# Optimization experiments

Hardware: AMD Instinct MI355X
Metric: run time of the kernel (lower is better)

Reference implementation:

```python
import jax, jax.numpy as jnp
import numpy as np

NEG_SLOPE = 0.2
EPS = 1e-16


def _add_self_loops(edge_index, edge_weight, N):
    # PyG add_self_loops with fill_value='mean': self-loop attr = mean of
    # incoming edge attrs per node (0 if node has no incoming edges).
    src, dst = edge_index[0], edge_index[1]
    ones = jnp.ones_like(edge_weight)
    cnt = jax.ops.segment_sum(ones, dst, num_segments=N)
    wsum = jax.ops.segment_sum(edge_weight, dst, num_segments=N)
    self_w = jnp.where(cnt > 0, wsum / jnp.maximum(cnt, 1.0), 0.0)
    loop = jnp.arange(N, dtype=src.dtype)
    return (jnp.concatenate([src, loop]), jnp.concatenate([dst, loop]),
            jnp.concatenate([edge_weight, self_w]))


def _gatv2_layer(x, src, dst, ew, Wl, Wr, att, We, bias, N):
    # x: [M, N, Din]; src/dst: [E']; ew: [E']; att: [H, C]
    M = x.shape[0]
    H, C = att.shape
    xl = (x @ Wl).reshape(M, N, H, C)   # source transform (lin_l)
    xr = (x @ Wr).reshape(M, N, H, C)   # target transform (lin_r)
    xj = xl[:, src]                      # [M, E', H, C] gather source feats
    xi = xr[:, dst]                      # [M, E', H, C] gather target feats
    ee = (ew[:, None] @ We).reshape(-1, H, C)  # [E', H, C] edge embedding
    s = jax.nn.leaky_relu(xi + xj + ee[None], NEG_SLOPE)
    logits = jnp.einsum('mehc,hc->meh', s, att)  # [M, E', H]
    # segment softmax over edges grouped by destination node
    smax = jax.vmap(lambda u: jax.ops.segment_max(u, dst, num_segments=N))(logits)
    a = jnp.exp(logits - smax[:, dst])
    denom = jax.vmap(lambda u: jax.ops.segment_sum(u, dst, num_segments=N))(a)
    alpha = a / (denom[:, dst] + EPS)
    msg = alpha[..., None] * xj          # [M, E', H, C]
    out = jax.vmap(lambda u: jax.ops.segment_sum(u, dst, num_segments=N))(msg)
    return out.reshape(M, N, H * C) + bias


def setup_inputs() -> dict:
    key = jax.random.key(0)
    ks = jax.random.split(key, 14)
    B, T, N, Din = 2, 8, 5000, 64
    E, H, OUT = 80000, 2, 128
    C = OUT // H  # 64
    g = jax.nn.initializers.glorot_uniform()
    inp = {
        'x': jax.random.normal(ks[0], (B, T, N, Din), jnp.float32),
        'edge_index': jax.random.randint(ks[1], (2, E), 0, N, jnp.int32),
        'edge_weight': jax.random.uniform(ks[2], (E,), jnp.float32),
        # conv1 params
        'Wl1': g(ks[3], (Din, H * C), jnp.float32),
        'Wr1': g(ks[4], (Din, H * C), jnp.float32),
        'att1': g(ks[5], (H, C), jnp.float32),
        'We1': g(ks[6], (1, H * C), jnp.float32),
        'b1': jnp.zeros((H * C,), jnp.float32),
        # conv2 params
        'Wl2': g(ks[7], (OUT, H * C), jnp.float32),
        'Wr2': g(ks[8], (OUT, H * C), jnp.float32),
        'att2': g(ks[9], (H, C), jnp.float32),
        'We2': g(ks[10], (1, H * C), jnp.float32),
        'b2': jnp.zeros((H * C,), jnp.float32),
    }
    return inp


def reference(x, edge_index, edge_weight, Wl1, Wr1, att1, We1, b1,
              Wl2, Wr2, att2, We2, b2):
    B, T, N, Din = x.shape
    M = B * T
    # Tiling edges by B*T with node offsets is equivalent to sharing the same
    # edge list across M independent graph copies -> vectorize over M.
    src, dst, ew = _add_self_loops(edge_index, edge_weight, N)
    h = x.reshape(M, N, Din)
    h = _gatv2_layer(h, src, dst, ew, Wl1, Wr1, att1, We1, b1, N)
    h = jax.nn.elu(h)
    h = _gatv2_layer(h, src, dst, ew, Wl2, Wr2, att2, We2, b2, N)
    h = jax.nn.elu(h)
    return h.reshape(B, T, N, -1)
```

## Files before the change

### kernel.cpp

```cpp
#include <hip/hip_runtime.h>
#include <cstdint>
#include <cstddef>

static constexpr float NEG_SLOPE_C = 0.2f;
static constexpr float EPS_C = 1e-16f;
static constexpr float LOG2E_C = 1.4426950408889634f;

#if defined(__has_builtin)
#if __has_builtin(__builtin_amdgcn_exp2f)
#define EXP2F(x) __builtin_amdgcn_exp2f(x)
#else
#define EXP2F(x) exp2f(x)
#endif
#else
#define EXP2F(x) exp2f(x)
#endif

typedef __attribute__((ext_vector_type(8))) short bf16x8;
typedef __attribute__((ext_vector_type(4))) float f32x4;

__device__ __forceinline__ short bf16_rne(float x) {
    unsigned u = __float_as_uint(x);
    u = (u + 0x7FFF + ((u >> 16) & 1)) >> 16;
    return (short)u;
}
__device__ __forceinline__ float bf16f(short s) {
    return __uint_as_float(((unsigned)(unsigned short)s) << 16);
}

template<int CTRL>
__device__ __forceinline__ float dpp_add_f(float v) {
    int x = __builtin_amdgcn_update_dpp(0, __float_as_int(v), CTRL, 0xf, 0xf, true);
    return v + __int_as_float(x);
}

__device__ __forceinline__ float reduce16(float q) {
    q = dpp_add_f<0xB1>(q);
    q = dpp_add_f<0x4E>(q);
    q = dpp_add_f<0x141>(q);
    q = dpp_add_f<0x140>(q);
    return q;
}


__global__ void degree_kernel(const int* __restrict__ ei, const float* __restrict__ ew,
                              int E, int* __restrict__ cnt, float* __restrict__ wsum) {
    int e = blockIdx.x * blockDim.x + threadIdx.x;
    if (e >= E) return;
    int dst = ei[E + e];
    atomicAdd(&cnt[dst], 1);
    atomicAdd(&wsum[dst], ew[e]);
}

__global__ void scan_kernel(const int* __restrict__ cnt, const float* __restrict__ wsum,
                            int N, int E, int* __restrict__ offs, float* __restrict__ self_w) {
    __shared__ int bufA[1024];
    __shared__ int bufB[1024];
    int t = threadIdx.x;
    int chunk = (N + 1023) / 1024;
    int lo = t * chunk;
    int hi = lo + chunk; if (hi > N) hi = N; if (lo > N) lo = N;
    int s = 0;
    for (int n = lo; n < hi; ++n) s += cnt[n];
    bufA[t] = s;
    __syncthreads();
    int* srcb = bufA; int* dstb = bufB;
    for (int d = 1; d < 1024; d <<= 1) {
        int v = srcb[t];
        if (t >= d) v += srcb[t - d];
        dstb[t] = v;
        __syncthreads();
        int* tmp = srcb; srcb = dstb; dstb = tmp;
    }
    int run = (t == 0) ? 0 : srcb[t - 1];
    for (int n = lo; n < hi; ++n) { offs[n] = run; run += cnt[n]; }
    if (t == 0) offs[N] = E;
    for (int n = t; n < N; n += 1024) {
        int c = cnt[n];
        self_w[n] = (c > 0) ? (wsum[n] / (float)c) : 0.0f;
    }
}

__global__ void scatter_kernel(const int* __restrict__ ei, const float* __restrict__ ew, int E,
                               const int* __restrict__ offs, int* __restrict__ cursor,
                               int2* __restrict__ pairs) {
    int e = blockIdx.x * blockDim.x + threadIdx.x;
    if (e >= E) return;
    int dst = ei[E + e];
    int pos = offs[dst] + atomicAdd(&cursor[dst], 1);
    pairs[pos] = make_int2(ei[e], __float_as_int(ew[e]));
}


template<int K>
__global__ void wprep_kernel(const float* __restrict__ Wl, const float* __restrict__ Wr,
                             uint4* __restrict__ Wf) {
    const int gid = blockIdx.x * 256 + threadIdx.x;
    const int lane = gid & 63;
    const int t = (gid >> 6) & 15;
    const int s = gid >> 10;
    const int mr = lane & 15, q = lane >> 4;
    const int col = t * 16 + mr;
    const float* src = (col < 128) ? (Wl + col) : (Wr + col - 128);
    union { short sh[8]; uint4 u; } hv, lv;
    #pragma unroll
    for (int j = 0; j < 8; ++j) {
        const float v = src[(size_t)(s * 32 + q * 8 + j) * 128];
        const short h = bf16_rne(v);
        hv.sh[j] = h;
        lv.sh[j] = bf16_rne(v - bf16f(h));
    }
    const size_t base = (size_t)s * 2048 + (size_t)(t * 2) * 64 + lane;
    Wf[base] = hv.u;
    Wf[base + 64] = lv.u;
}


template<int K>
__global__ __launch_bounds__(256) void gemm_mfma_kernel(
    const float* __restrict__ X, const uint4* __restrict__ Wf,
    float* __restrict__ outL, float* __restrict__ outR) {
    __shared__ uint4 wbuf[2048];
    const int tid = threadIdx.x;
    const int wv = tid >> 6;
    const int lane = tid & 63;
    const int q = lane >> 4;
    const int mr = lane & 15;
    const int xrow = blockIdx.x * 64 + wv * 16 + mr;

    f32x4 acc[16];
    #pragma unroll
    for (int t = 0; t < 16; ++t) acc[t] = (f32x4){0.f, 0.f, 0.f, 0.f};

    const float* xp = X + (size_t)xrow * K + q * 8;

    for (int s = 0; s < K / 32; ++s) {
        const float4 a0 = *(const float4*)(xp + s * 32);
        const float4 a1 = *(const float4*)(xp + s * 32 + 4);

        __syncthreads();
        const uint4* gsrc = Wf + (size_t)s * 2048 + wv * 512 + lane;
        #pragma unroll
        for (int i = 0; i < 8; ++i)
            wbuf[wv * 512 + i * 64 + lane] = gsrc[i * 64];
        __syncthreads();

        const float av[8] = {a0.x, a0.y, a0.z, a0.w, a1.x, a1.y, a1.z, a1.w};
        bf16x8 xh, xl;
        #pragma unroll
        for (int j = 0; j < 8; ++j) {
            const short h = bf16_rne(av[j]);
            xh[j] = h;
            xl[j] = bf16_rne(av[j] - bf16f(h));
        }
        #pragma unroll
        for (int t = 0; t < 16; ++t) {
            const bf16x8 wh = *(const bf16x8*)&wbuf[(t * 2) * 64 + lane];
            const bf16x8 wl = *(const bf16x8*)&wbuf[(t * 2 + 1) * 64 + lane];
            acc[t] = __builtin_amdgcn_mfma_f32_16x16x32_bf16(wh, xh, acc[t], 0, 0, 0);
            acc[t] = __builtin_amdgcn_mfma_f32_16x16x32_bf16(wl, xh, acc[t], 0, 0, 0);
            acc[t] = __builtin_amdgcn_mfma_f32_16x16x32_bf16(wh, xl, acc[t], 0, 0, 0);
        }
    }

    const size_t ob = (size_t)xrow * 128 + q * 4;
    #pragma unroll
    for (int t = 0; t < 8; ++t) {
        *(float4*)(outL + ob + t * 16) =
            make_float4(acc[t][0], acc[t][1], acc[t][2], acc[t][3]);
        *(float4*)(outR + ob + t * 16) =
            make_float4(acc[t + 8][0], acc[t + 8][1], acc[t + 8][2], acc[t + 8][3]);
    }
}


__global__ __launch_bounds__(256) void edge_kernel(
    const float* __restrict__ xl, const float* __restrict__ xr,
    const int* __restrict__ offs, const int2* __restrict__ pairs,
    const float* __restrict__ self_w,
    const float* __restrict__ att, const float* __restrict__ We,
    const float* __restrict__ bias, float* __restrict__ out,
    int N, int M) {
    const int wave = __builtin_amdgcn_readfirstlane(threadIdx.x >> 6);
    const int b = blockIdx.x;
    const int hb = (b >= 10000) ? (b - 10000) : b;
    const int m = ((b >= 10000) ? 8 : 0) + (hb & 7);
    const int n = (hb >> 3) * 4 + wave;
    if (n >= N) return;
    const int lane = threadIdx.x & 63;
    const int j = lane & 31;
    const bool hi = lane >= 32;

    const float4* xlm4 = (const float4*)(xl + (size_t)m * N * 128);
    const float4* xrm4 = (const float4*)(xr + (size_t)m * N * 128);

    float4 att4 = ((const float4*)att)[j];
    att4.x *= LOG2E_C; att4.y *= LOG2E_C; att4.z *= LOG2E_C; att4.w *= LOG2E_C;
    const float4 we4 = ((const float4*)We)[j];
    const float4 xi4 = xrm4[n * 32 + j];

    float base, lsum;
    float4 acc;
    {
        const float sw = self_w[n];
        const float4 xj = xlm4[n * 32 + j];
        float s0 = fmaf(sw, we4.x, xi4.x) + xj.x;
        float s1 = fmaf(sw, we4.y, xi4.y) + xj.y;
        float s2 = fmaf(sw, we4.z, xi4.z) + xj.z;
        float s3 = fmaf(sw, we4.w, xi4.w) + xj.w;
        s0 = fmaf(NEG_SLOPE_C - 1.0f, fminf(s0, 0.f), s0);
        s1 = fmaf(NEG_SLOPE_C - 1.0f, fminf(s1, 0.f), s1);
        s2 = fmaf(NEG_SLOPE_C - 1.0f, fminf(s2, 0.f), s2);
        s3 = fmaf(NEG_SLOPE_C - 1.0f, fminf(s3, 0.f), s3);
        float q = s0 * att4.x;
        q = fmaf(s1, att4.y, q);
        q = fmaf(s2, att4.z, q);
        q = fmaf(s3, att4.w, q);
        base = reduce16(q);
        lsum = 0.5f;
        acc = make_float4(xj.x * 0.5f, xj.y * 0.5f, xj.z * 0.5f, xj.w * 0.5f);
    }

    const int beg = offs[n], end = offs[n + 1];
    int e = beg;
    #pragma unroll 2
    for (; e + 2 <= end; e += 2) {
        const int2 prA = pairs[e];
        const int2 prB = pairs[e + 1];
        const int src = hi ? prB.x : prA.x;
        const float w = __int_as_float(hi ? prB.y : prA.y);
        const float4 xj = xlm4[src * 32 + j];
        float s0 = fmaf(w, we4.x, xi4.x) + xj.x;
        float s1 = fmaf(w, we4.y, xi4.y) + xj.y;
        float s2 = fmaf(w, we4.z, xi4.z) + xj.z;
        float s3 = fmaf(w, we4.w, xi4.w) + xj.w;
        s0 = fmaf(NEG_SLOPE_C - 1.0f, fminf(s0, 0.f), s0);
        s1 = fmaf(NEG_SLOPE_C - 1.0f, fminf(s1, 0.f), s1);
        s2 = fmaf(NEG_SLOPE_C - 1.0f, fminf(s2, 0.f), s2);
        s3 = fmaf(NEG_SLOPE_C - 1.0f, fminf(s3, 0.f), s3);
        float q = s0 * att4.x;
        q = fmaf(s1, att4.y, q);
        q = fmaf(s2, att4.z, q);
        q = fmaf(s3, att4.w, q);
        q = reduce16(q);
        const float t = EXP2F(q - base);
        lsum += t;
        acc.x = fmaf(t, xj.x, acc.x);
        acc.y = fmaf(t, xj.y, acc.y);
        acc.z = fmaf(t, xj.z, acc.z);
        acc.w = fmaf(t, xj.w, acc.w);
    }
    if (e < end) {
        const int2 pr = pairs[e];
        const int src = pr.x;
        const float w = __int_as_float(pr.y);
        const float4 xj = xlm4[src * 32 + j];
        float s0 = fmaf(w, we4.x, xi4.x) + xj.x;
        float s1 = fmaf(w, we4.y, xi4.y) + xj.y;
        float s2 = fmaf(w, we4.z, xi4.z) + xj.z;
        float s3 = fmaf(w, we4.w, xi4.w) + xj.w;
        s0 = fmaf(NEG_SLOPE_C - 1.0f, fminf(s0, 0.f), s0);
        s1 = fmaf(NEG_SLOPE_C - 1.0f, fminf(s1, 0.f), s1);
        s2 = fmaf(NEG_SLOPE_C - 1.0f, fminf(s2, 0.f), s2);
        s3 = fmaf(NEG_SLOPE_C - 1.0f, fminf(s3, 0.f), s3);
        float q = s0 * att4.x;
        q = fmaf(s1, att4.y, q);
        q = fmaf(s2, att4.z, q);
        q = fmaf(s3, att4.w, q);
        q = reduce16(q);
        float t = EXP2F(q - base);
        t = hi ? 0.f : t;
        lsum += t;
        acc.x = fmaf(t, xj.x, acc.x);
        acc.y = fmaf(t, xj.y, acc.y);
        acc.z = fmaf(t, xj.z, acc.z);
        acc.w = fmaf(t, xj.w, acc.w);
    }

    lsum += __shfl_xor(lsum, 32, 64);
    acc.x += __shfl_xor(acc.x, 32, 64);
    acc.y += __shfl_xor(acc.y, 32, 64);
    acc.z += __shfl_xor(acc.z, 32, 64);
    acc.w += __shfl_xor(acc.w, 32, 64);

    const float inv = 1.f / (lsum + EPS_C);
    const float4 b4 = ((const float4*)bias)[j];
    float o0 = fmaf(acc.x, inv, b4.x);
    float o1 = fmaf(acc.y, inv, b4.y);
    float o2 = fmaf(acc.z, inv, b4.z);
    float o3 = fmaf(acc.w, inv, b4.w);
    o0 = o0 > 0.f ? o0 : (__expf(o0) - 1.f);
    o1 = o1 > 0.f ? o1 : (__expf(o1) - 1.f);
    o2 = o2 > 0.f ? o2 : (__expf(o2) - 1.f);
    o3 = o3 > 0.f ? o3 : (__expf(o3) - 1.f);
    if (!hi) {
        ((float4*)(out + (size_t)m * N * 128))[n * 32 + j] =
            make_float4(o0, o1, o2, o3);
    }
}


extern "C" void kernel_launch(void* const* d_in, const int* in_sizes, int n_in,
                              void* d_out, int out_size, void* d_ws, size_t ws_size,
                              hipStream_t stream) {
    const float* x    = (const float*)d_in[0];
    const int*   ei   = (const int*)d_in[1];
    const float* ew   = (const float*)d_in[2];
    const float* Wl1  = (const float*)d_in[3];
    const float* Wr1  = (const float*)d_in[4];
    const float* att1 = (const float*)d_in[5];
    const float* We1  = (const float*)d_in[6];
    const float* b1   = (const float*)d_in[7];
    const float* Wl2  = (const float*)d_in[8];
    const float* Wr2  = (const float*)d_in[9];
    const float* att2 = (const float*)d_in[10];
    const float* We2  = (const float*)d_in[11];
    const float* b2   = (const float*)d_in[12];

    const int E = in_sizes[1] / 2;
    const int N = 5000;
    const int R = out_size / 128;
    const int M = R / N;

    char* ws = (char*)d_ws;
    size_t off = 0;
    auto alloc = [&](size_t bytes) {
        char* p = ws + off;
        off = (off + bytes + 255) & ~(size_t)255;
        return p;
    };
    int*   cnt    = (int*)  alloc((size_t)N * 4);
    float* wsum   = (float*)alloc((size_t)N * 4);
    float* selfw  = (float*)alloc((size_t)N * 4);
    int*   offs   = (int*)  alloc((size_t)(N + 1) * 4);
    int*   cursor = (int*)  alloc((size_t)N * 4);
    int2*  pairs  = (int2*) alloc((size_t)E * 8);
    uint4* wf1    = (uint4*)alloc((size_t)2 * 2048 * 16);
    uint4* wf2    = (uint4*)alloc((size_t)4 * 2048 * 16);
    float* bufA   = (float*)alloc((size_t)R * 128 * 4);
    float* bufB   = (float*)alloc((size_t)R * 128 * 4);
    float* bufC   = (float*)alloc((size_t)R * 128 * 4);

    hipMemsetAsync(cnt,    0, (size_t)N * 4, stream);
    hipMemsetAsync(wsum,   0, (size_t)N * 4, stream);
    hipMemsetAsync(cursor, 0, (size_t)N * 4, stream);

    int eb = (E + 255) / 256;
    degree_kernel<<<eb, 256, 0, stream>>>(ei, ew, E, cnt, wsum);
    scan_kernel<<<1, 1024, 0, stream>>>(cnt, wsum, N, E, offs, selfw);
    scatter_kernel<<<eb, 256, 0, stream>>>(ei, ew, E, offs, cursor, pairs);
    wprep_kernel<64><<<8, 256, 0, stream>>>(Wl1, Wr1, wf1);
    wprep_kernel<128><<<16, 256, 0, stream>>>(Wl2, Wr2, wf2);

    const int gb = R / 64;
    const int tb = 2 * ((N + 3) / 4) * 8;

    gemm_mfma_kernel<64><<<gb, 256, 0, stream>>>(x, wf1, bufA, bufB);
    edge_kernel<<<tb, 256, 0, stream>>>(bufA, bufB, offs, pairs, selfw,
                                        att1, We1, b1, bufC, N, M);
    gemm_mfma_kernel<128><<<gb, 256, 0, stream>>>(bufC, wf2, bufA, bufB);
    edge_kernel<<<tb, 256, 0, stream>>>(bufA, bufB, offs, pairs, selfw,
                                        att2, We2, b2, (float*)d_out, N, M);
}
```

Before: 301.9 us.

## Process four edges per wave with eight channels per lane and pair prefetch

The edge aggregation kernel now splits each 64-lane wave into four 16-lane groups. Each group handles a different edge at once, and each lane covers eight channels instead of four. Leaky-ReLU is rewritten as 0.6*s + 0.4*|s| folded into pre-scaled attention vectors, and the next edge pair is prefetched one iteration ahead. The aim is to halve loop trips per node and cut the per-edge instruction count. In exchange, each lane holds more registers, the tail needs masking, and the final reductions need more cross-lane shuffles.

Measured after the change: 336.0 us. +11.3%, slower.

```diff
diff --git a/kernel.cpp b/kernel.cpp
--- a/kernel.cpp
+++ b/kernel.cpp
@@ -34,11 +34,10 @@
     return v + __int_as_float(x);
 }
 
-__device__ __forceinline__ float reduce16(float q) {
+__device__ __forceinline__ float reduce8(float q) {
     q = dpp_add_f<0xB1>(q);
     q = dpp_add_f<0x4E>(q);
     q = dpp_add_f<0x141>(q);
-    q = dpp_add_f<0x140>(q);
     return q;
 }
 
@@ -188,114 +187,142 @@
     const int n = (hb >> 3) * 4 + wave;
     if (n >= N) return;
     const int lane = threadIdx.x & 63;
-    const int j = lane & 31;
-    const bool hi = lane >= 32;
+    const int j = lane & 15;
+    const int g = lane >> 4;
 
     const float4* xlm4 = (const float4*)(xl + (size_t)m * N * 128);
     const float4* xrm4 = (const float4*)(xr + (size_t)m * N * 128);
 
-    float4 att4 = ((const float4*)att)[j];
-    att4.x *= LOG2E_C; att4.y *= LOG2E_C; att4.z *= LOG2E_C; att4.w *= LOG2E_C;
-    const float4 we4 = ((const float4*)We)[j];
-    const float4 xi4 = xrm4[n * 32 + j];
+    float a06[8], a04[8], we_[8], xi_[8];
+    {
+        const float4 atA = ((const float4*)att)[2 * j];
+        const float4 atB = ((const float4*)att)[2 * j + 1];
+        const float4 weA = ((const float4*)We)[2 * j];
+        const float4 weB = ((const float4*)We)[2 * j + 1];
+        const float4 xiA = xrm4[(size_t)n * 32 + 2 * j];
+        const float4 xiB = xrm4[(size_t)n * 32 + 2 * j + 1];
+        const float at[8] = {atA.x, atA.y, atA.z, atA.w, atB.x, atB.y, atB.z, atB.w};
+        const float we8[8] = {weA.x, weA.y, weA.z, weA.w, weB.x, weB.y, weB.z, weB.w};
+        const float xi8[8] = {xiA.x, xiA.y, xiA.z, xiA.w, xiB.x, xiB.y, xiB.z, xiB.w};
+        #pragma unroll
+        for (int k = 0; k < 8; ++k) {
+            a06[k] = at[k] * (0.6f * LOG2E_C);
+            a04[k] = at[k] * (0.4f * LOG2E_C);
+            we_[k] = we8[k];
+            xi_[k] = xi8[k];
+        }
+    }
 
     float base, lsum;
-    float4 acc;
+    float acc[8];
     {
         const float sw = self_w[n];
-        const float4 xj = xlm4[n * 32 + j];
-        float s0 = fmaf(sw, we4.x, xi4.x) + xj.x;
-        float s1 = fmaf(sw, we4.y, xi4.y) + xj.y;
-        float s2 = fmaf(sw, we4.z, xi4.z) + xj.z;
-        float s3 = fmaf(sw, we4.w, xi4.w) + xj.w;
-        s0 = fmaf(NEG_SLOPE_C - 1.0f, fminf(s0, 0.f), s0);
-        s1 = fmaf(NEG_SLOPE_C - 1.0f, fminf(s1, 0.f), s1);
-        s2 = fmaf(NEG_SLOPE_C - 1.0f, fminf(s2, 0.f), s2);
-        s3 = fmaf(NEG_SLOPE_C - 1.0f, fminf(s3, 0.f), s3);
-        float q = s0 * att4.x;
-        q = fmaf(s1, att4.y, q);
-        q = fmaf(s2, att4.z, q);
-        q = fmaf(s3, att4.w, q);
-        base = reduce16(q);
-        lsum = 0.5f;
-        acc = make_float4(xj.x * 0.5f, xj.y * 0.5f, xj.z * 0.5f, xj.w * 0.5f);
+        const float4 xjA = xlm4[(size_t)n * 32 + 2 * j];
+        const float4 xjB = xlm4[(size_t)n * 32 + 2 * j + 1];
+        const float xj[8] = {xjA.x, xjA.y, xjA.z, xjA.w, xjB.x, xjB.y, xjB.z, xjB.w};
+        float q0 = 0.f, q1 = 0.f;
+        #pragma unroll
+        for (int k = 0; k < 4; ++k) {
+            const float s = fmaf(sw, we_[k], xi_[k]) + xj[k];
+            q0 = fmaf(a06[k], s, q0);
+            q0 = fmaf(a04[k], fabsf(s), q0);
+        }
+        #pragma unroll
+        for (int k = 4; k < 8; ++k) {
+            const float s = fmaf(sw, we_[k], xi_[k]) + xj[k];
+            q1 = fmaf(a06[k], s, q1);
+            q1 = fmaf(a04[k], fabsf(s), q1);
+        }
+        base = reduce8(q0 + q1);
+        lsum = 0.25f;
+        #pragma unroll
+        for (int k = 0; k < 8; ++k) acc[k] = 0.25f * xj[k];
     }
 
     const int beg = offs[n], end = offs[n + 1];
-    int e = beg;
-    #pragma unroll 2
-    for (; e + 2 <= end; e += 2) {
-        const int2 prA = pairs[e];
-        const int2 prB = pairs[e + 1];
-        const int src = hi ? prB.x : prA.x;
-        const float w = __int_as_float(hi ? prB.y : prA.y);
-        const float4 xj = xlm4[src * 32 + j];
-        float s0 = fmaf(w, we4.x, xi4.x) + xj.x;
-        float s1 = fmaf(w, we4.y, xi4.y) + xj.y;
-        float s2 = fmaf(w, we4.z, xi4.z) + xj.z;
-        float s3 = fmaf(w, we4.w, xi4.w) + xj.w;
-        s0 = fmaf(NEG_SLOPE_C - 1.0f, fminf(s0, 0.f), s0);
-        s1 = fmaf(NEG_SLOPE_C - 1.0f, fminf(s1, 0.f), s1);
-        s2 = fmaf(NEG_SLOPE_C - 1.0f, fminf(s2, 0.f), s2);
-        s3 = fmaf(NEG_SLOPE_C - 1.0f, fminf(s3, 0.f), s3);
-        float q = s0 * att4.x;
-        q = fmaf(s1, att4.y, q);
-        q = fmaf(s2, att4.z, q);
-        q = fmaf(s3, att4.w, q);
-        q = reduce16(q);
-        const float t = EXP2F(q - base);
-        lsum += t;
-        acc.x = fmaf(t, xj.x, acc.x);
-        acc.y = fmaf(t, xj.y, acc.y);
-        acc.z = fmaf(t, xj.z, acc.z);
-        acc.w = fmaf(t, xj.w, acc.w);
-    }
-    if (e < end) {
-        const int2 pr = pairs[e];
-        const int src = pr.x;
-        const float w = __int_as_float(pr.y);
-        const float4 xj = xlm4[src * 32 + j];
-        float s0 = fmaf(w, we4.x, xi4.x) + xj.x;
-        float s1 = fmaf(w, we4.y, xi4.y) + xj.y;
-        float s2 = fmaf(w, we4.z, xi4.z) + xj.z;
-        float s3 = fmaf(w, we4.w, xi4.w) + xj.w;
-        s0 = fmaf(NEG_SLOPE_C - 1.0f, fminf(s0, 0.f), s0);
-        s1 = fmaf(NEG_SLOPE_C - 1.0f, fminf(s1, 0.f), s1);
-        s2 = fmaf(NEG_SLOPE_C - 1.0f, fminf(s2, 0.f), s2);
-        s3 = fmaf(NEG_SLOPE_C - 1.0f, fminf(s3, 0.f), s3);
-        float q = s0 * att4.x;
-        q = fmaf(s1, att4.y, q);
-        q = fmaf(s2, att4.z, q);
-        q = fmaf(s3, att4.w, q);
-        q = reduce16(q);
-        float t = EXP2F(q - base);
-        t = hi ? 0.f : t;
-        lsum += t;
-        acc.x = fmaf(t, xj.x, acc.x);
-        acc.y = fmaf(t, xj.y, acc.y);
-        acc.z = fmaf(t, xj.z, acc.z);
-        acc.w = fmaf(t, xj.w, acc.w);
-    }
-
+    if (end > beg) {
+        const int last = end - 1;
+        int e = beg;
+        int2 pr = pairs[min(e + g, last)];
+        while (e + 4 <= end) {
+            const int2 cur = pr;
+            const int en = e + 4;
+            pr = pairs[min(en + g, last)];
+            const int src = cur.x;
+            const float w = __int_as_float(cur.y);
+            const float4 xjA = xlm4[(size_t)src * 32 + 2 * j];
+            const float4 xjB = xlm4[(size_t)src * 32 + 2 * j + 1];
+            const float xj[8] = {xjA.x, xjA.y, xjA.z, xjA.w, xjB.x, xjB.y, xjB.z, xjB.w};
+            float q0 = 0.f, q1 = 0.f;
+            #pragma unroll
+            for (int k = 0; k < 4; ++k) {
+                const float s = fmaf(w, we_[k], xi_[k]) + xj[k];
+                q0 = fmaf(a06[k], s, q0);
+                q0 = fmaf(a04[k], fabsf(s), q0);
+            }
+            #pragma unroll
+            for (int k = 4; k < 8; ++k) {
+                const float s = fmaf(w, we_[k], xi_[k]) + xj[k];
+                q1 = fmaf(a06[k], s, q1);
+                q1 = fmaf(a04[k], fabsf(s), q1);
+            }
+            const float q = reduce8(q0 + q1);
+            const float t = EXP2F(q - base);
+            lsum += t;
+            #pragma unroll
+            for (int k = 0; k < 8; ++k) acc[k] = fmaf(t, xj[k], acc[k]);
+            e = en;
+        }
+        if (e < end) {
+            const int src = pr.x;
+            const float w = __int_as_float(pr.y);
+            const float4 xjA = xlm4[(size_t)src * 32 + 2 * j];
+            const float4 xjB = xlm4[(size_t)src * 32 + 2 * j + 1];
+            const float xj[8] = {xjA.x, xjA.y, xjA.z, xjA.w, xjB.x, xjB.y, xjB.z, xjB.w};
+            float q0 = 0.f, q1 = 0.f;
+            #pragma unroll
+            for (int k = 0; k < 4; ++k) {
+                const float s = fmaf(w, we_[k], xi_[k]) + xj[k];
+                q0 = fmaf(a06[k], s, q0);
+                q0 = fmaf(a04[k], fabsf(s), q0);
+            }
+            #pragma unroll
+            for (int k = 4; k < 8; ++k) {
+                const float s = fmaf(w, we_[k], xi_[k]) + xj[k];
+                q1 = fmaf(a06[k], s, q1);
+                q1 = fmaf(a04[k], fabsf(s), q1);
+            }
+            const float q = reduce8(q0 + q1);
+            float t = EXP2F(q - base);
+            t = (e + g <= last) ? t : 0.f;
+            lsum += t;
+            #pragma unroll
+            for (int k = 0; k < 8; ++k) acc[k] = fmaf(t, xj[k], acc[k]);
+        }
+    }
+
+    lsum += __shfl_xor(lsum, 16, 64);
     lsum += __shfl_xor(lsum, 32, 64);
-    acc.x += __shfl_xor(acc.x, 32, 64);
-    acc.y += __shfl_xor(acc.y, 32, 64);
-    acc.z += __shfl_xor(acc.z, 32, 64);
-    acc.w += __shfl_xor(acc.w, 32, 64);
+    #pragma unroll
+    for (int k = 0; k < 8; ++k) {
+        acc[k] += __shfl_xor(acc[k], 16, 64);
+        acc[k] += __shfl_xor(acc[k], 32, 64);
+    }
 
     const float inv = 1.f / (lsum + EPS_C);
-    const float4 b4 = ((const float4*)bias)[j];
-    float o0 = fmaf(acc.x, inv, b4.x);
-    float o1 = fmaf(acc.y, inv, b4.y);
-    float o2 = fmaf(acc.z, inv, b4.z);
-    float o3 = fmaf(acc.w, inv, b4.w);
-    o0 = o0 > 0.f ? o0 : (__expf(o0) - 1.f);
-    o1 = o1 > 0.f ? o1 : (__expf(o1) - 1.f);
-    o2 = o2 > 0.f ? o2 : (__expf(o2) - 1.f);
-    o3 = o3 > 0.f ? o3 : (__expf(o3) - 1.f);
-    if (!hi) {
-        ((float4*)(out + (size_t)m * N * 128))[n * 32 + j] =
-            make_float4(o0, o1, o2, o3);
+    const float4 bA = ((const float4*)bias)[2 * j];
+    const float4 bB = ((const float4*)bias)[2 * j + 1];
+    const float bb[8] = {bA.x, bA.y, bA.z, bA.w, bB.x, bB.y, bB.z, bB.w};
+    float o[8];
+    #pragma unroll
+    for (int k = 0; k < 8; ++k) {
+        float v = fmaf(acc[k], inv, bb[k]);
+        o[k] = v > 0.f ? v : (__expf(v) - 1.f);
+    }
+    if (g == 0) {
+        float4* op = (float4*)(out + (size_t)m * N * 128);
+        op[(size_t)n * 32 + 2 * j] = make_float4(o[0], o[1], o[2], o[3]);
+        op[(size_t)n * 32 + 2 * j + 1] = make_float4(o[4], o[5], o[6], o[7]);
     }
 }
 
```

## Use packed FP32 math and abs-form leaky ReLU in GATv2 edge kernel

Applied to the files above, without the earlier changes.

Rewrites the per-edge score computation with v_pk_add/mul/fma_f32 on float pairs and expresses leaky ReLU as 0.6*s + 0.4*|s|, folding both constants and log2e into the attention weights. Edge pairs are widened to 16-byte records that hold a premultiplied byte offset for the source row and a duplicated weight, so each half-wave loads its edge with one vector load and needs no select or index multiply. The aim is fewer VALU instructions in the edge loop. The cost is twice the pair storage and bandwidth, plus inline asm that limits compiler scheduling.

New measurement: 339.9 us. 1.13x slower.

```diff
diff --git a/kernel.cpp b/kernel.cpp
--- a/kernel.cpp
+++ b/kernel.cpp
@@ -18,6 +18,29 @@
 
 typedef __attribute__((ext_vector_type(8))) short bf16x8;
 typedef __attribute__((ext_vector_type(4))) float f32x4;
+typedef __attribute__((ext_vector_type(2))) float f32x2;
+
+__device__ __forceinline__ f32x2 pk_add(f32x2 a, f32x2 b) {
+    f32x2 d;
+    asm("v_pk_add_f32 %0, %1, %2" : "=v"(d) : "v"(a), "v"(b));
+    return d;
+}
+__device__ __forceinline__ f32x2 pk_mul(f32x2 a, f32x2 b) {
+    f32x2 d;
+    asm("v_pk_mul_f32 %0, %1, %2" : "=v"(d) : "v"(a), "v"(b));
+    return d;
+}
+__device__ __forceinline__ f32x2 pk_fma(f32x2 a, f32x2 b, f32x2 c) {
+    f32x2 d;
+    asm("v_pk_fma_f32 %0, %1, %2, %3" : "=v"(d) : "v"(a), "v"(b), "v"(c));
+    return d;
+}
+__device__ __forceinline__ f32x2 pk_abs(f32x2 a) {
+    f32x2 d;
+    d.x = __builtin_fabsf(a.x);
+    d.y = __builtin_fabsf(a.y);
+    return d;
+}
 
 __device__ __forceinline__ short bf16_rne(float x) {
     unsigned u = __float_as_uint(x);
@@ -83,12 +106,13 @@
 
 __global__ void scatter_kernel(const int* __restrict__ ei, const float* __restrict__ ew, int E,
                                const int* __restrict__ offs, int* __restrict__ cursor,
-                               int2* __restrict__ pairs) {
+                               int4* __restrict__ pairs) {
     int e = blockIdx.x * blockDim.x + threadIdx.x;
     if (e >= E) return;
     int dst = ei[E + e];
     int pos = offs[dst] + atomicAdd(&cursor[dst], 1);
-    pairs[pos] = make_int2(ei[e], __float_as_int(ew[e]));
+    int wb = __float_as_int(ew[e]);
+    pairs[pos] = make_int4(ei[e] * 512, 0, wb, wb);
 }
 
 
@@ -176,7 +200,7 @@
 
 __global__ __launch_bounds__(256) void edge_kernel(
     const float* __restrict__ xl, const float* __restrict__ xr,
-    const int* __restrict__ offs, const int2* __restrict__ pairs,
+    const int* __restrict__ offs, const int4* __restrict__ pairs,
     const float* __restrict__ self_w,
     const float* __restrict__ att, const float* __restrict__ We,
     const float* __restrict__ bias, float* __restrict__ out,
@@ -190,91 +214,84 @@
     const int lane = threadIdx.x & 63;
     const int j = lane & 31;
     const bool hi = lane >= 32;
-
-    const float4* xlm4 = (const float4*)(xl + (size_t)m * N * 128);
-    const float4* xrm4 = (const float4*)(xr + (size_t)m * N * 128);
-
-    float4 att4 = ((const float4*)att)[j];
-    att4.x *= LOG2E_C; att4.y *= LOG2E_C; att4.z *= LOG2E_C; att4.w *= LOG2E_C;
-    const float4 we4 = ((const float4*)We)[j];
-    const float4 xi4 = xrm4[n * 32 + j];
+    const int hio = (lane >> 5) << 4;
+    const int j16 = j << 4;
+
+    const char* xlp = (const char*)(xl + (size_t)m * N * 128);
+    const char* xrp = (const char*)(xr + (size_t)m * N * 128);
+
+    f32x2 a06_01, a06_23, a04_01, a04_23, we01, we23, xi01, xi23;
+    {
+        const float4 at4 = ((const float4*)att)[j];
+        const float4 we4 = ((const float4*)We)[j];
+        const float4 xi4 = *(const float4*)(xrp + (size_t)n * 512 + j16);
+        const float c06 = 0.6f * LOG2E_C, c04 = 0.4f * LOG2E_C;
+        a06_01 = (f32x2){at4.x * c06, at4.y * c06};
+        a06_23 = (f32x2){at4.z * c06, at4.w * c06};
+        a04_01 = (f32x2){at4.x * c04, at4.y * c04};
+        a04_23 = (f32x2){at4.z * c04, at4.w * c04};
+        we01 = (f32x2){we4.x, we4.y};
+        we23 = (f32x2){we4.z, we4.w};
+        xi01 = (f32x2){xi4.x, xi4.y};
+        xi23 = (f32x2){xi4.z, xi4.w};
+    }
 
     float base, lsum;
     float4 acc;
     {
         const float sw = self_w[n];
-        const float4 xj = xlm4[n * 32 + j];
-        float s0 = fmaf(sw, we4.x, xi4.x) + xj.x;
-        float s1 = fmaf(sw, we4.y, xi4.y) + xj.y;
-        float s2 = fmaf(sw, we4.z, xi4.z) + xj.z;
-        float s3 = fmaf(sw, we4.w, xi4.w) + xj.w;
-        s0 = fmaf(NEG_SLOPE_C - 1.0f, fminf(s0, 0.f), s0);
-        s1 = fmaf(NEG_SLOPE_C - 1.0f, fminf(s1, 0.f), s1);
-        s2 = fmaf(NEG_SLOPE_C - 1.0f, fminf(s2, 0.f), s2);
-        s3 = fmaf(NEG_SLOPE_C - 1.0f, fminf(s3, 0.f), s3);
-        float q = s0 * att4.x;
-        q = fmaf(s1, att4.y, q);
-        q = fmaf(s2, att4.z, q);
-        q = fmaf(s3, att4.w, q);
-        base = reduce16(q);
+        const f32x2 sw2 = (f32x2){sw, sw};
+        const float4 xj4 = *(const float4*)(xlp + (size_t)n * 512 + j16);
+        const f32x2 s01 = pk_fma(sw2, we01, pk_add(xi01, (f32x2){xj4.x, xj4.y}));
+        const f32x2 s23 = pk_fma(sw2, we23, pk_add(xi23, (f32x2){xj4.z, xj4.w}));
+        f32x2 qp = pk_mul(a06_01, s01);
+        qp = pk_fma(a04_01, pk_abs(s01), qp);
+        qp = pk_fma(a06_23, s23, qp);
+        qp = pk_fma(a04_23, pk_abs(s23), qp);
+        base = reduce16(qp.x + qp.y);
         lsum = 0.5f;
-        acc = make_float4(xj.x * 0.5f, xj.y * 0.5f, xj.z * 0.5f, xj.w * 0.5f);
+        acc = make_float4(xj4.x * 0.5f, xj4.y * 0.5f, xj4.z * 0.5f, xj4.w * 0.5f);
     }
 
     const int beg = offs[n], end = offs[n + 1];
     int e = beg;
     #pragma unroll 2
     for (; e + 2 <= end; e += 2) {
-        const int2 prA = pairs[e];
-        const int2 prB = pairs[e + 1];
-        const int src = hi ? prB.x : prA.x;
-        const float w = __int_as_float(hi ? prB.y : prA.y);
-        const float4 xj = xlm4[src * 32 + j];
-        float s0 = fmaf(w, we4.x, xi4.x) + xj.x;
-        float s1 = fmaf(w, we4.y, xi4.y) + xj.y;
-        float s2 = fmaf(w, we4.z, xi4.z) + xj.z;
-        float s3 = fmaf(w, we4.w, xi4.w) + xj.w;
-        s0 = fmaf(NEG_SLOPE_C - 1.0f, fminf(s0, 0.f), s0);
-        s1 = fmaf(NEG_SLOPE_C - 1.0f, fminf(s1, 0.f), s1);
-        s2 = fmaf(NEG_SLOPE_C - 1.0f, fminf(s2, 0.f), s2);
-        s3 = fmaf(NEG_SLOPE_C - 1.0f, fminf(s3, 0.f), s3);
-        float q = s0 * att4.x;
-        q = fmaf(s1, att4.y, q);
-        q = fmaf(s2, att4.z, q);
-        q = fmaf(s3, att4.w, q);
-        q = reduce16(q);
+        const int4 pr = *(const int4*)((const char*)pairs + ((size_t)e << 4) + hio);
+        const f32x2 w2 = (f32x2){__int_as_float(pr.z), __int_as_float(pr.w)};
+        const float4 xj4 = *(const float4*)(xlp + (unsigned)(pr.x + j16));
+        const f32x2 s01 = pk_fma(w2, we01, pk_add(xi01, (f32x2){xj4.x, xj4.y}));
+        const f32x2 s23 = pk_fma(w2, we23, pk_add(xi23, (f32x2){xj4.z, xj4.w}));
+        f32x2 qp = pk_mul(a06_01, s01);
+        qp = pk_fma(a04_01, pk_abs(s01), qp);
+        qp = pk_fma(a06_23, s23, qp);
+        qp = pk_fma(a04_23, pk_abs(s23), qp);
+        const float q = reduce16(qp.x + qp.y);
         const float t = EXP2F(q - base);
         lsum += t;
-        acc.x = fmaf(t, xj.x, acc.x);
-        acc.y = fmaf(t, xj.y, acc.y);
-        acc.z = fmaf(t, xj.z, acc.z);
-        acc.w = fmaf(t, xj.w, acc.w);
+        acc.x = fmaf(t, xj4.x, acc.x);
+        acc.y = fmaf(t, xj4.y, acc.y);
+        acc.z = fmaf(t, xj4.z, acc.z);
+        acc.w = fmaf(t, xj4.w, acc.w);
     }
     if (e < end) {
-        const int2 pr = pairs[e];
-        const int src = pr.x;
-        const float w = __int_as_float(pr.y);
-        const float4 xj = xlm4[src * 32 + j];
-        float s0 = fmaf(w, we4.x, xi4.x) + xj.x;
-        float s1 = fmaf(w, we4.y, xi4.y) + xj.y;
-        float s2 = fmaf(w, we4.z, xi4.z) + xj.z;
-        float s3 = fmaf(w, we4.w, xi4.w) + xj.w;
-        s0 = fmaf(NEG_SLOPE_C - 1.0f, fminf(s0, 0.f), s0);
-        s1 = fmaf(NEG_SLOPE_C - 1.0f, fminf(s1, 0.f), s1);
-        s2 = fmaf(NEG_SLOPE_C - 1.0f, fminf(s2, 0.f), s2);
-        s3 = fmaf(NEG_SLOPE_C - 1.0f, fminf(s3, 0.f), s3);
-        float q = s0 * att4.x;
-        q = fmaf(s1, att4.y, q);
-        q = fmaf(s2, att4.z, q);
-        q = fmaf(s3, att4.w, q);
-        q = reduce16(q);
+        const int4 pr = *(const int4*)((const char*)pairs + ((size_t)e << 4));
+        const f32x2 w2 = (f32x2){__int_as_float(pr.z), __int_as_float(pr.w)};
+        const float4 xj4 = *(const float4*)(xlp + (unsigned)(pr.x + j16));
+        const f32x2 s01 = pk_fma(w2, we01, pk_add(xi01, (f32x2){xj4.x, xj4.y}));
+        const f32x2 s23 = pk_fma(w2, we23, pk_add(xi23, (f32x2){xj4.z, xj4.w}));
+        f32x2 qp = pk_mul(a06_01, s01);
+        qp = pk_fma(a04_01, pk_abs(s01), qp);
+        qp = pk_fma(a06_23, s23, qp);
+        qp = pk_fma(a04_23, pk_abs(s23), qp);
+        const float q = reduce16(qp.x + qp.y);
         float t = EXP2F(q - base);
         t = hi ? 0.f : t;
         lsum += t;
-        acc.x = fmaf(t, xj.x, acc.x);
-        acc.y = fmaf(t, xj.y, acc.y);
-        acc.z = fmaf(t, xj.z, acc.z);
-        acc.w = fmaf(t, xj.w, acc.w);
+        acc.x = fmaf(t, xj4.x, acc.x);
+        acc.y = fmaf(t, xj4.y, acc.y);
+        acc.z = fmaf(t, xj4.z, acc.z);
+        acc.w = fmaf(t, xj4.w, acc.w);
     }
 
     lsum += __shfl_xor(lsum, 32, 64);
@@ -334,7 +351,7 @@
     float* selfw  = (float*)alloc((size_t)N * 4);
     int*   offs   = (int*)  alloc((size_t)(N + 1) * 4);
     int*   cursor = (int*)  alloc((size_t)N * 4);
-    int2*  pairs  = (int2*) alloc((size_t)E * 8);
+    int4*  pairs  = (int4*) alloc((size_t)(E + 1) * 16);
     uint4* wf1    = (uint4*)alloc((size_t)2 * 2048 * 16);
     uint4* wf2    = (uint4*)alloc((size_t)4 * 2048 * 16);
     float* bufA   = (float*)alloc((size_t)R * 128 * 4);
```
